# Kernel optimization log

Measured on AMD Instinct MI355X. Metric: run time of the kernel, lower is better.

The kernel has to match this reference:

```python
import jax, jax.numpy as jnp
import numpy as np

# dims: B=4 batch, S=2048 seq, D=4096 in, O=4096 out, E=16 adapters, R=16 rank

def setup_inputs() -> dict:
    key = jax.random.key(0)
    k = jax.random.split(key, 6)
    x = jax.random.normal(k[0], (4, 2048, 4096), jnp.float32)
    W = jax.random.normal(k[1], (4096, 4096), jnp.float32) * 0.02   # base_linear.weight [O, D]
    bias = jax.random.normal(k[2], (4096,), jnp.float32) * 0.02
    A = jax.random.normal(k[3], (16, 16, 4096), jnp.float32) * 0.02  # stacked a_factors [E, R, D]
    Bf = jax.random.normal(k[4], (16, 4096, 16), jnp.float32) * 0.02 # stacked b_factors [E, O, R]
    coeffs = jax.random.uniform(k[5], (16,), jnp.float32)            # task coefficients per adapter
    scales = jnp.full((16,), 0.5, jnp.float32)                       # per-adapter static scales
    return {"x": x, "W": W, "bias": bias, "A": A, "Bf": Bf, "coeffs": coeffs, "scales": scales}

def reference(x, W, bias, A, Bf, coeffs, scales):
    # base: out = x @ W.T + bias
    out = jnp.einsum('bsd,od->bso', x, W) + bias
    # fused LoRA: sum_e coeffs[e]*scales[e] * (x @ A[e].T) @ Bf[e].T
    xa = jnp.einsum('bsd,erd->ebsr', x, A)          # [E, B, S, R] (small: R=16)
    w = coeffs * scales                               # [E]
    upd = jnp.einsum('ebsr,eor,e->bso', xa, Bf, w)  # weighted accumulate over adapters
    return out + upd
```

## Files before the change

### kernel.cpp

```cpp
#include <hip/hip_runtime.h>

typedef float f32x4 __attribute__((ext_vector_type(4)));
typedef __bf16 bf16x8 __attribute__((ext_vector_type(8)));
typedef unsigned short u16x8 __attribute__((ext_vector_type(8)));

__device__ __forceinline__ unsigned short f2bf(float f) {
  union { float f; unsigned int u; } v; v.f = f;
  unsigned int u = v.u;
  unsigned int r = (u + 0x7FFFu + ((u >> 16) & 1u)) >> 16;
  return (unsigned short)r;
}

__global__ __launch_bounds__(256) void k_cast_bf16(const float* __restrict__ in,
                                                   unsigned short* __restrict__ out, int n8) {
  const f32x4* p = (const f32x4*)in;
  for (int i = blockIdx.x * 256 + threadIdx.x; i < n8; i += 2048 * 256) {
    f32x4 a = p[2 * i], b = p[2 * i + 1];
    u16x8 o;
    o[0] = f2bf(a[0]); o[1] = f2bf(a[1]); o[2] = f2bf(a[2]); o[3] = f2bf(a[3]);
    o[4] = f2bf(b[0]); o[5] = f2bf(b[1]); o[6] = f2bf(b[2]); o[7] = f2bf(b[3]);
    ((u16x8*)out)[i] = o;
  }
}

__global__ void k_build_bw(const float* __restrict__ Bf,
                           const float* __restrict__ coeffs,
                           const float* __restrict__ scales,
                           unsigned short* __restrict__ bw) {
  int t = blockIdx.x * 256 + threadIdx.x;
  int o = t >> 8, k = t & 255, e = k >> 4, r = k & 15;
  float v = coeffs[e] * scales[e] * Bf[((size_t)e * 4096 + o) * 16 + r];
  bw[t] = f2bf(v);
}

__global__ void k_build_at(const float* __restrict__ A,
                           unsigned short* __restrict__ at) {
  __shared__ float tile[64][65];
  int kt = blockIdx.x * 64, dt = blockIdx.y * 64;
  int tx = threadIdx.x & 63, ty = threadIdx.x >> 6;
#pragma unroll
  for (int j = 0; j < 64; j += 4)
    tile[ty + j][tx] = A[(size_t)(kt + ty + j) * 4096 + dt + tx];
  __syncthreads();
#pragma unroll
  for (int j = 0; j < 64; j += 4)
    at[(size_t)(dt + ty + j) * 256 + kt + tx] = f2bf(tile[tx][ty + j]);
}

template <int M_, int N_, int K_>
__global__ __launch_bounds__(256) void k_gemm_prep(
    const unsigned short* __restrict__ Abuf,
    const unsigned short* __restrict__ Bbuf,
    const float* __restrict__ Wadd,
    unsigned short* __restrict__ outB) {
  constexpr int NBN = N_ / 128;
  constexpr int NWG = (M_ / 128) * NBN;
  const int bid = blockIdx.x;
  const int swz = (bid & 7) * (NWG / 8) + (bid >> 3);
  const int bm = swz / NBN, bn = swz % NBN;

  __shared__ unsigned short ldsA[128 * 64];
  __shared__ unsigned short ldsB[128 * 64];

  const int t = threadIdx.x, w = t >> 6, l = t & 63;
  const int wr = w >> 1, wc = w & 1;

  f32x4 acc[4][4] = {};
  const int m0 = bm * 128, n0 = bn * 128;
  const int srow = w * 8 + (l >> 3);
  const int scol = (l & 7) * 8;
  const unsigned short* gA = Abuf + (size_t)(m0 + srow) * K_ + scol;
  const unsigned short* gB = Bbuf + (size_t)(n0 + srow) * K_ + scol;

  for (int kt = 0; kt < K_; kt += 64) {
#pragma unroll
    for (int i = 0; i < 4; ++i) {
      __builtin_amdgcn_global_load_lds(
          (__attribute__((address_space(1))) void*)(gA + (size_t)i * 32 * K_ + kt),
          (__attribute__((address_space(3))) void*)(ldsA + i * 2048 + w * 512), 16, 0, 0);
      __builtin_amdgcn_global_load_lds(
          (__attribute__((address_space(1))) void*)(gB + (size_t)i * 32 * K_ + kt),
          (__attribute__((address_space(3))) void*)(ldsB + i * 2048 + w * 512), 16, 0, 0);
    }
    __syncthreads();
#pragma unroll
    for (int kk = 0; kk < 2; ++kk) {
      const int col = kk * 32 + (l >> 4) * 8;
      const int arow = wr * 64 + (l & 15);
      const int brow = wc * 64 + (l & 15);
      bf16x8 af[4], bfv[4];
#pragma unroll
      for (int mi = 0; mi < 4; ++mi)
        af[mi] = *(const bf16x8*)&ldsA[(arow + mi * 16) * 64 + col];
#pragma unroll
      for (int ni = 0; ni < 4; ++ni)
        bfv[ni] = *(const bf16x8*)&ldsB[(brow + ni * 16) * 64 + col];
#pragma unroll
      for (int mi = 0; mi < 4; ++mi)
#pragma unroll
        for (int ni = 0; ni < 4; ++ni)
          acc[mi][ni] = __builtin_amdgcn_mfma_f32_16x16x32_bf16(
              af[mi], bfv[ni], acc[mi][ni], 0, 0, 0);
    }
    __syncthreads();
  }

  const int mrow0 = m0 + wr * 64 + (l >> 4) * 4;
  const int ncol0 = n0 + wc * 64 + (l & 15);
#pragma unroll
  for (int mi = 0; mi < 4; ++mi)
#pragma unroll
    for (int r = 0; r < 4; ++r) {
      const int m = mrow0 + mi * 16 + r;
#pragma unroll
      for (int ni = 0; ni < 4; ++ni) {
        const int n = ncol0 + ni * 16;
        outB[(size_t)m * N_ + n] = f2bf(acc[mi][ni][r] + Wadd[(size_t)m * N_ + n]);
      }
    }
}

template <int M_, int N_, int K_>
__global__ __launch_bounds__(512, 2) void k_gemm256(
    const unsigned short* __restrict__ Abuf,
    const unsigned short* __restrict__ Bbuf,
    const float* __restrict__ bias,
    float* __restrict__ outF) {
  constexpr int NBN = N_ / 256;
  constexpr int NWG = (M_ / 256) * NBN;
  constexpr int NT = K_ / 32;
  static_assert(NWG % 8 == 0, "bijective xcd swizzle");
  static_assert(NT % 2 == 0 && NT >= 6, "pipeline depth");

  const int bid = blockIdx.x;
  const int swz = (bid & 7) * (NWG / 8) + (bid >> 3);
  const int bm = swz / NBN, bn = swz % NBN;
  const int m0 = bm * 256, n0 = bn * 256;

  __shared__ __attribute__((aligned(128))) unsigned short lds[81920];
  char* ldsb = (char*)lds;

  const int tid = threadIdx.x, w = tid >> 6, l = tid & 63;
  const int wr = w >> 2, wc = w & 3;

  const int scol = ((l & 3) ^ ((l >> 3) & 3)) * 8;
  const unsigned short* gA = Abuf + (size_t)(m0 + w * 16 + (l >> 2)) * K_ + scol;
  const unsigned short* gB = Bbuf + (size_t)(n0 + w * 16 + (l >> 2)) * K_ + scol;
  const int dA = w * 1024;
  const int dB = 16384 + w * 1024;

  const int qp = ((l >> 4) ^ ((l >> 1) & 3)) << 4;
  const int raOff = (wr * 128 + (l & 15)) * 64 + qp;
  const int rbOff = 16384 + (wc * 64 + (l & 15)) * 64 + qp;

  f32x4 acc[8][4] = {};

#define STAGE_T(tt, bf)                                                               \
  do {                                                                                \
    const int bb_ = (bf) * 32768;                                                     \
    const size_t ko_ = (size_t)(tt) * 32;                                             \
    _Pragma("unroll") for (int i_ = 0; i_ < 2; ++i_) {                                \
      __builtin_amdgcn_global_load_lds(                                               \
          (__attribute__((address_space(1))) void*)(gA + (size_t)i_ * 128 * K_ + ko_),\
          (__attribute__((address_space(3))) void*)(ldsb + bb_ + i_ * 8192 + dA),     \
          16, 0, 0);                                                                  \
      __builtin_amdgcn_global_load_lds(                                               \
          (__attribute__((address_space(1))) void*)(gB + (size_t)i_ * 128 * K_ + ko_),\
          (__attribute__((address_space(3))) void*)(ldsb + bb_ + i_ * 8192 + dB),     \
          16, 0, 0);                                                                  \
    }                                                                                 \
  } while (0)

#define RD_A(mi, bf) (*(const bf16x8*)(ldsb + (bf) * 32768 + raOff + (mi) * 1024))
#define RD_B(ni, bf) (*(const bf16x8*)(ldsb + (bf) * 32768 + rbOff + (ni) * 1024))

#define TILE_BODY(bf, stg_t, stg_b, do_stg)                                           \
  do {                                                                                \
    bf16x8 fa0 = RD_A(0, bf), fa1 = RD_A(1, bf), fa2 = RD_A(2, bf), fa3 = RD_A(3, bf);\
    bf16x8 fa4 = RD_A(4, bf), fa5 = RD_A(5, bf), fa6 = RD_A(6, bf), fa7 = RD_A(7, bf);\
    bf16x8 fb0 = RD_B(0, bf), fb1 = RD_B(1, bf), fb2 = RD_B(2, bf), fb3 = RD_B(3, bf);\
    if (do_stg) STAGE_T(stg_t, stg_b);                                                \
    __builtin_amdgcn_s_setprio(1);                                                    \
    _Pragma("unroll") for (int ni_ = 0; ni_ < 4; ++ni_) {                             \
      bf16x8 vv = (ni_ == 0) ? fb0 : (ni_ == 1) ? fb1 : (ni_ == 2) ? fb2 : fb3;       \
      acc[0][ni_] = __builtin_amdgcn_mfma_f32_16x16x32_bf16(fa0, vv, acc[0][ni_], 0, 0, 0); \
      acc[1][ni_] = __builtin_amdgcn_mfma_f32_16x16x32_bf16(fa1, vv, acc[1][ni_], 0, 0, 0); \
      acc[2][ni_] = __builtin_amdgcn_mfma_f32_16x16x32_bf16(fa2, vv, acc[2][ni_], 0, 0, 0); \
      acc[3][ni_] = __builtin_amdgcn_mfma_f32_16x16x32_bf16(fa3, vv, acc[3][ni_], 0, 0, 0); \
      acc[4][ni_] = __builtin_amdgcn_mfma_f32_16x16x32_bf16(fa4, vv, acc[4][ni_], 0, 0, 0); \
      acc[5][ni_] = __builtin_amdgcn_mfma_f32_16x16x32_bf16(fa5, vv, acc[5][ni_], 0, 0, 0); \
      acc[6][ni_] = __builtin_amdgcn_mfma_f32_16x16x32_bf16(fa6, vv, acc[6][ni_], 0, 0, 0); \
      acc[7][ni_] = __builtin_amdgcn_mfma_f32_16x16x32_bf16(fa7, vv, acc[7][ni_], 0, 0, 0); \
    }                                                                                 \
    __builtin_amdgcn_s_setprio(0);                                                    \
  } while (0)

  STAGE_T(0, 0); STAGE_T(1, 1); STAGE_T(2, 2);

  int bT = 0;
  for (int tt = 0; tt < NT; tt += 2) {
    const int b0 = bT;
    const int b1 = (bT + 1 >= 5) ? bT + 1 - 5 : bT + 1;
    const int s3 = (bT + 3 >= 5) ? bT + 3 - 5 : bT + 3;
    const int s4 = (bT + 4 >= 5) ? bT + 4 - 5 : bT + 4;
    const bool st3 = (tt + 3) < NT, st4 = (tt + 4) < NT;

    if (tt + 2 < NT) asm volatile("s_waitcnt vmcnt(4)" ::: "memory");
    else             asm volatile("s_waitcnt vmcnt(0)" ::: "memory");
    __builtin_amdgcn_s_barrier();
    __builtin_amdgcn_sched_barrier(0);

    if ((w & 1) == 0) {
      TILE_BODY(b0, tt + 3, s3, st3);
      TILE_BODY(b1, tt + 4, s4, st4);
    } else {
      TILE_BODY(b1, tt + 3, s3, st3);
      TILE_BODY(b0, tt + 4, s4, st4);
    }

    bT += 2; if (bT >= 5) bT -= 5;
  }
#undef STAGE_T
#undef RD_A
#undef RD_B
#undef TILE_BODY

#pragma unroll
  for (int ni = 0; ni < 4; ++ni) {
    const int n = n0 + wc * 64 + ni * 16 + (l & 15);
    const float bv2 = bias[n];
#pragma unroll
    for (int mi = 0; mi < 8; ++mi) {
      const int m = m0 + wr * 128 + mi * 16 + (l >> 4) * 4;
#pragma unroll
      for (int r = 0; r < 4; ++r)
        outF[(size_t)(m + r) * N_ + n] = acc[mi][ni][r] + bv2;
    }
  }
}

extern "C" void kernel_launch(void* const* d_in, const int* in_sizes, int n_in,
                              void* d_out, int out_size, void* d_ws, size_t ws_size,
                              hipStream_t stream) {
  const float* x      = (const float*)d_in[0];
  const float* W      = (const float*)d_in[1];
  const float* bias   = (const float*)d_in[2];
  const float* A      = (const float*)d_in[3];
  const float* Bf     = (const float*)d_in[4];
  const float* coeffs = (const float*)d_in[5];
  const float* scales = (const float*)d_in[6];
  float* out = (float*)d_out;

  char* ws = (char*)d_ws;
  unsigned short* xb   = (unsigned short*)(ws);
  unsigned short* weff = (unsigned short*)(ws + 67108864);
  unsigned short* bw   = (unsigned short*)(ws + 67108864 + 33554432);
  unsigned short* at   = (unsigned short*)(ws + 67108864 + 33554432 + 2097152);

  k_cast_bf16<<<2048, 256, 0, stream>>>(x, xb, (8192 * 4096) / 8);
  k_build_bw<<<4096, 256, 0, stream>>>(Bf, coeffs, scales, bw);
  k_build_at<<<dim3(4, 64), 256, 0, stream>>>(A, at);
  k_gemm_prep<4096, 4096, 256><<<1024, 256, 0, stream>>>(bw, at, W, weff);
  k_gemm256<8192, 4096, 4096><<<512, 512, 0, stream>>>(xb, weff, bias, out);
}
```

Before: 352.3 us.

## Software-pipeline LDS fragment reads against MFMA groups within the K loop

Each tile's compute is split into two MFMA half-groups (low and high A rows), and the LDS fragment reads for the next half are interleaved with the MFMAs of the previous half. The second half of each tile is carried across the barrier into the next iteration, with a prologue and an epilogue added. Scheduling barriers pin this order. The aim is to hide LDS read latency behind matrix-core work instead of loading all fragments before any MFMA. The per-wave odd/even tile order swap is removed, and extra fragment registers are held live, which may raise register pressure at two waves per SIMD.

```diff
diff --git a/kernel.cpp b/kernel.cpp
--- a/kernel.cpp
+++ b/kernel.cpp
@@ -130,7 +130,7 @@
   constexpr int NWG = (M_ / 256) * NBN;
   constexpr int NT = K_ / 32;
   static_assert(NWG % 8 == 0, "bijective xcd swizzle");
-  static_assert(NT % 2 == 0 && NT >= 6, "pipeline depth");
+  static_assert(NT % 2 == 0 && NT >= 8, "pipeline depth");
 
   const int bid = blockIdx.x;
   const int swz = (bid & 7) * (NWG / 8) + (bid >> 3);
@@ -154,6 +154,7 @@
   const int rbOff = 16384 + (wc * 64 + (l & 15)) * 64 + qp;
 
   f32x4 acc[8][4] = {};
+  bf16x8 faL[4], faH[4], fbX[4], fbY[4];
 
 #define STAGE_T(tt, bf)                                                               \
   do {                                                                                \
@@ -173,57 +174,99 @@
 
 #define RD_A(mi, bf) (*(const bf16x8*)(ldsb + (bf) * 32768 + raOff + (mi) * 1024))
 #define RD_B(ni, bf) (*(const bf16x8*)(ldsb + (bf) * 32768 + rbOff + (ni) * 1024))
-
-#define TILE_BODY(bf, stg_t, stg_b, do_stg)                                           \
-  do {                                                                                \
-    bf16x8 fa0 = RD_A(0, bf), fa1 = RD_A(1, bf), fa2 = RD_A(2, bf), fa3 = RD_A(3, bf);\
-    bf16x8 fa4 = RD_A(4, bf), fa5 = RD_A(5, bf), fa6 = RD_A(6, bf), fa7 = RD_A(7, bf);\
-    bf16x8 fb0 = RD_B(0, bf), fb1 = RD_B(1, bf), fb2 = RD_B(2, bf), fb3 = RD_B(3, bf);\
-    if (do_stg) STAGE_T(stg_t, stg_b);                                                \
-    __builtin_amdgcn_s_setprio(1);                                                    \
-    _Pragma("unroll") for (int ni_ = 0; ni_ < 4; ++ni_) {                             \
-      bf16x8 vv = (ni_ == 0) ? fb0 : (ni_ == 1) ? fb1 : (ni_ == 2) ? fb2 : fb3;       \
-      acc[0][ni_] = __builtin_amdgcn_mfma_f32_16x16x32_bf16(fa0, vv, acc[0][ni_], 0, 0, 0); \
-      acc[1][ni_] = __builtin_amdgcn_mfma_f32_16x16x32_bf16(fa1, vv, acc[1][ni_], 0, 0, 0); \
-      acc[2][ni_] = __builtin_amdgcn_mfma_f32_16x16x32_bf16(fa2, vv, acc[2][ni_], 0, 0, 0); \
-      acc[3][ni_] = __builtin_amdgcn_mfma_f32_16x16x32_bf16(fa3, vv, acc[3][ni_], 0, 0, 0); \
-      acc[4][ni_] = __builtin_amdgcn_mfma_f32_16x16x32_bf16(fa4, vv, acc[4][ni_], 0, 0, 0); \
-      acc[5][ni_] = __builtin_amdgcn_mfma_f32_16x16x32_bf16(fa5, vv, acc[5][ni_], 0, 0, 0); \
-      acc[6][ni_] = __builtin_amdgcn_mfma_f32_16x16x32_bf16(fa6, vv, acc[6][ni_], 0, 0, 0); \
-      acc[7][ni_] = __builtin_amdgcn_mfma_f32_16x16x32_bf16(fa7, vv, acc[7][ni_], 0, 0, 0); \
-    }                                                                                 \
-    __builtin_amdgcn_s_setprio(0);                                                    \
+#define SB __builtin_amdgcn_sched_barrier(0)
+
+#define ALPHA(bf, FB)                                                                 \
+  do {                                                                               \
+    faL[0] = RD_A(0, bf); faL[1] = RD_A(1, bf);                                      \
+    faL[2] = RD_A(2, bf); faL[3] = RD_A(3, bf);                                      \
+    FB[0] = RD_B(0, bf); FB[1] = RD_B(1, bf);                                        \
+    FB[2] = RD_B(2, bf); FB[3] = RD_B(3, bf);                                        \
+    SB;                                                                              \
+  } while (0)
+
+#define BETA(bf, stg_t, stg_b, do_stg)                                               \
+  do {                                                                               \
+    faH[0] = RD_A(4, bf); faH[1] = RD_A(5, bf);                                      \
+    faH[2] = RD_A(6, bf); faH[3] = RD_A(7, bf);                                      \
+    if (do_stg) STAGE_T(stg_t, stg_b);                                               \
+    SB;                                                                              \
+  } while (0)
+
+#define G1(FB)                                                                       \
+  do {                                                                               \
+    __builtin_amdgcn_s_setprio(1);                                                   \
+    _Pragma("unroll") for (int ni_ = 0; ni_ < 4; ++ni_) {                            \
+      acc[0][ni_] = __builtin_amdgcn_mfma_f32_16x16x32_bf16(faL[0], FB[ni_], acc[0][ni_], 0, 0, 0); \
+      acc[1][ni_] = __builtin_amdgcn_mfma_f32_16x16x32_bf16(faL[1], FB[ni_], acc[1][ni_], 0, 0, 0); \
+      acc[2][ni_] = __builtin_amdgcn_mfma_f32_16x16x32_bf16(faL[2], FB[ni_], acc[2][ni_], 0, 0, 0); \
+      acc[3][ni_] = __builtin_amdgcn_mfma_f32_16x16x32_bf16(faL[3], FB[ni_], acc[3][ni_], 0, 0, 0); \
+    }                                                                                \
+    __builtin_amdgcn_s_setprio(0);                                                   \
+    SB;                                                                              \
+  } while (0)
+
+#define G2(FB)                                                                       \
+  do {                                                                               \
+    __builtin_amdgcn_s_setprio(1);                                                   \
+    _Pragma("unroll") for (int ni_ = 0; ni_ < 4; ++ni_) {                            \
+      acc[4][ni_] = __builtin_amdgcn_mfma_f32_16x16x32_bf16(faH[0], FB[ni_], acc[4][ni_], 0, 0, 0); \
+      acc[5][ni_] = __builtin_amdgcn_mfma_f32_16x16x32_bf16(faH[1], FB[ni_], acc[5][ni_], 0, 0, 0); \
+      acc[6][ni_] = __builtin_amdgcn_mfma_f32_16x16x32_bf16(faH[2], FB[ni_], acc[6][ni_], 0, 0, 0); \
+      acc[7][ni_] = __builtin_amdgcn_mfma_f32_16x16x32_bf16(faH[3], FB[ni_], acc[7][ni_], 0, 0, 0); \
+    }                                                                                \
+    __builtin_amdgcn_s_setprio(0);                                                   \
+    SB;                                                                              \
+  } while (0)
+
+#define TOPWAIT(cond)                                                                \
+  do {                                                                               \
+    if (cond) asm volatile("s_waitcnt vmcnt(4)" ::: "memory");                       \
+    else      asm volatile("s_waitcnt vmcnt(0)" ::: "memory");                       \
+    __builtin_amdgcn_s_barrier();                                                    \
+    SB;                                                                              \
   } while (0)
 
   STAGE_T(0, 0); STAGE_T(1, 1); STAGE_T(2, 2);
 
-  int bT = 0;
-  for (int tt = 0; tt < NT; tt += 2) {
+  TOPWAIT(2 < NT);
+  ALPHA(0, fbX);
+  BETA(0, 3, 3, 3 < NT);
+  G1(fbX);
+  ALPHA(1, fbY);
+  G2(fbX);
+  BETA(1, 4, 4, 4 < NT);
+  G1(fbY);
+
+  int bT = 2;
+  for (int tt = 2; tt < NT; tt += 2) {
     const int b0 = bT;
     const int b1 = (bT + 1 >= 5) ? bT + 1 - 5 : bT + 1;
     const int s3 = (bT + 3 >= 5) ? bT + 3 - 5 : bT + 3;
     const int s4 = (bT + 4 >= 5) ? bT + 4 - 5 : bT + 4;
-    const bool st3 = (tt + 3) < NT, st4 = (tt + 4) < NT;
-
-    if (tt + 2 < NT) asm volatile("s_waitcnt vmcnt(4)" ::: "memory");
-    else             asm volatile("s_waitcnt vmcnt(0)" ::: "memory");
-    __builtin_amdgcn_s_barrier();
-    __builtin_amdgcn_sched_barrier(0);
-
-    if ((w & 1) == 0) {
-      TILE_BODY(b0, tt + 3, s3, st3);
-      TILE_BODY(b1, tt + 4, s4, st4);
-    } else {
-      TILE_BODY(b1, tt + 3, s3, st3);
-      TILE_BODY(b0, tt + 4, s4, st4);
-    }
+
+    TOPWAIT(tt + 2 < NT);
+    ALPHA(b0, fbX);
+    G2(fbY);
+    BETA(b0, tt + 3, s3, (tt + 3) < NT);
+    G1(fbX);
+    ALPHA(b1, fbY);
+    G2(fbX);
+    BETA(b1, tt + 4, s4, (tt + 4) < NT);
+    G1(fbY);
 
     bT += 2; if (bT >= 5) bT -= 5;
   }
+  G2(fbY);
 #undef STAGE_T
 #undef RD_A
 #undef RD_B
-#undef TILE_BODY
+#undef SB
+#undef ALPHA
+#undef BETA
+#undef G1
+#undef G2
+#undef TOPWAIT
 
 #pragma unroll
   for (int ni = 0; ni < 4; ++ni) {
```

Measured after the change: 346.0 us. Within noise of the previous version (-1.8%).

## Run main GEMM with 16 waves per block and merge small prep kernels

Applied to the files above, without the earlier changes.

The 256x256 GEMM block now uses 1024 threads (16 waves in a 4x4 grid), and each wave computes a 64x64 sub-tile instead of 128x64. Staging needs one load per matrix per thread, and the wait count and per-wave buffer ordering are adjusted to match. The intent is more waves to hide latency and fewer accumulator registers per wave, at the cost of extra LDS fragment reads per MFMA and lower occupancy per CU. The x cast becomes one element-group per thread instead of a grid-stride loop, and the Bw and A-transpose prep kernels are merged into one launch to cut launch overhead.

```diff
diff --git a/kernel.cpp b/kernel.cpp
--- a/kernel.cpp
+++ b/kernel.cpp
@@ -13,38 +13,40 @@
 
 __global__ __launch_bounds__(256) void k_cast_bf16(const float* __restrict__ in,
                                                    unsigned short* __restrict__ out, int n8) {
+  int i = blockIdx.x * 256 + threadIdx.x;
+  if (i >= n8) return;
   const f32x4* p = (const f32x4*)in;
-  for (int i = blockIdx.x * 256 + threadIdx.x; i < n8; i += 2048 * 256) {
-    f32x4 a = p[2 * i], b = p[2 * i + 1];
-    u16x8 o;
-    o[0] = f2bf(a[0]); o[1] = f2bf(a[1]); o[2] = f2bf(a[2]); o[3] = f2bf(a[3]);
-    o[4] = f2bf(b[0]); o[5] = f2bf(b[1]); o[6] = f2bf(b[2]); o[7] = f2bf(b[3]);
-    ((u16x8*)out)[i] = o;
-  }
-}
-
-__global__ void k_build_bw(const float* __restrict__ Bf,
-                           const float* __restrict__ coeffs,
-                           const float* __restrict__ scales,
-                           unsigned short* __restrict__ bw) {
-  int t = blockIdx.x * 256 + threadIdx.x;
-  int o = t >> 8, k = t & 255, e = k >> 4, r = k & 15;
-  float v = coeffs[e] * scales[e] * Bf[((size_t)e * 4096 + o) * 16 + r];
-  bw[t] = f2bf(v);
-}
-
-__global__ void k_build_at(const float* __restrict__ A,
-                           unsigned short* __restrict__ at) {
+  f32x4 a = p[2 * i], b = p[2 * i + 1];
+  u16x8 o;
+  o[0] = f2bf(a[0]); o[1] = f2bf(a[1]); o[2] = f2bf(a[2]); o[3] = f2bf(a[3]);
+  o[4] = f2bf(b[0]); o[5] = f2bf(b[1]); o[6] = f2bf(b[2]); o[7] = f2bf(b[3]);
+  ((u16x8*)out)[i] = o;
+}
+
+__global__ void k_build_bwat(const float* __restrict__ Bf,
+                             const float* __restrict__ coeffs,
+                             const float* __restrict__ scales,
+                             const float* __restrict__ A,
+                             unsigned short* __restrict__ bw,
+                             unsigned short* __restrict__ at) {
   __shared__ float tile[64][65];
-  int kt = blockIdx.x * 64, dt = blockIdx.y * 64;
-  int tx = threadIdx.x & 63, ty = threadIdx.x >> 6;
-#pragma unroll
-  for (int j = 0; j < 64; j += 4)
-    tile[ty + j][tx] = A[(size_t)(kt + ty + j) * 4096 + dt + tx];
-  __syncthreads();
-#pragma unroll
-  for (int j = 0; j < 64; j += 4)
-    at[(size_t)(dt + ty + j) * 256 + kt + tx] = f2bf(tile[tx][ty + j]);
+  if (blockIdx.x < 4096) {
+    int t = blockIdx.x * 256 + threadIdx.x;
+    int o = t >> 8, k = t & 255, e = k >> 4, r = k & 15;
+    float v = coeffs[e] * scales[e] * Bf[((size_t)e * 4096 + o) * 16 + r];
+    bw[t] = f2bf(v);
+  } else {
+    int b = blockIdx.x - 4096;
+    int kt = (b & 3) * 64, dt = (b >> 2) * 64;
+    int tx = threadIdx.x & 63, ty = threadIdx.x >> 6;
+#pragma unroll
+    for (int j = 0; j < 64; j += 4)
+      tile[ty + j][tx] = A[(size_t)(kt + ty + j) * 4096 + dt + tx];
+    __syncthreads();
+#pragma unroll
+    for (int j = 0; j < 64; j += 4)
+      at[(size_t)(dt + ty + j) * 256 + kt + tx] = f2bf(tile[tx][ty + j]);
+  }
 }
 
 template <int M_, int N_, int K_>
@@ -121,7 +123,7 @@
 }
 
 template <int M_, int N_, int K_>
-__global__ __launch_bounds__(512, 2) void k_gemm256(
+__global__ __launch_bounds__(1024) void k_gemm256(
     const unsigned short* __restrict__ Abuf,
     const unsigned short* __restrict__ Bbuf,
     const float* __restrict__ bias,
@@ -150,25 +152,21 @@
   const int dB = 16384 + w * 1024;
 
   const int qp = ((l >> 4) ^ ((l >> 1) & 3)) << 4;
-  const int raOff = (wr * 128 + (l & 15)) * 64 + qp;
+  const int raOff = (wr * 64 + (l & 15)) * 64 + qp;
   const int rbOff = 16384 + (wc * 64 + (l & 15)) * 64 + qp;
 
-  f32x4 acc[8][4] = {};
+  f32x4 acc[4][4] = {};
 
 #define STAGE_T(tt, bf)                                                               \
   do {                                                                                \
     const int bb_ = (bf) * 32768;                                                     \
     const size_t ko_ = (size_t)(tt) * 32;                                             \
-    _Pragma("unroll") for (int i_ = 0; i_ < 2; ++i_) {                                \
-      __builtin_amdgcn_global_load_lds(                                               \
-          (__attribute__((address_space(1))) void*)(gA + (size_t)i_ * 128 * K_ + ko_),\
-          (__attribute__((address_space(3))) void*)(ldsb + bb_ + i_ * 8192 + dA),     \
-          16, 0, 0);                                                                  \
-      __builtin_amdgcn_global_load_lds(                                               \
-          (__attribute__((address_space(1))) void*)(gB + (size_t)i_ * 128 * K_ + ko_),\
-          (__attribute__((address_space(3))) void*)(ldsb + bb_ + i_ * 8192 + dB),     \
-          16, 0, 0);                                                                  \
-    }                                                                                 \
+    __builtin_amdgcn_global_load_lds(                                                 \
+        (__attribute__((address_space(1))) void*)(gA + ko_),                          \
+        (__attribute__((address_space(3))) void*)(ldsb + bb_ + dA), 16, 0, 0);        \
+    __builtin_amdgcn_global_load_lds(                                                 \
+        (__attribute__((address_space(1))) void*)(gB + ko_),                          \
+        (__attribute__((address_space(3))) void*)(ldsb + bb_ + dB), 16, 0, 0);        \
   } while (0)
 
 #define RD_A(mi, bf) (*(const bf16x8*)(ldsb + (bf) * 32768 + raOff + (mi) * 1024))
@@ -176,21 +174,17 @@
 
 #define TILE_BODY(bf, stg_t, stg_b, do_stg)                                           \
   do {                                                                                \
-    bf16x8 fa0 = RD_A(0, bf), fa1 = RD_A(1, bf), fa2 = RD_A(2, bf), fa3 = RD_A(3, bf);\
-    bf16x8 fa4 = RD_A(4, bf), fa5 = RD_A(5, bf), fa6 = RD_A(6, bf), fa7 = RD_A(7, bf);\
-    bf16x8 fb0 = RD_B(0, bf), fb1 = RD_B(1, bf), fb2 = RD_B(2, bf), fb3 = RD_B(3, bf);\
+    bf16x8 fa[4], fb[4];                                                              \
+    _Pragma("unroll") for (int i_ = 0; i_ < 4; ++i_) {                                \
+      fa[i_] = RD_A(i_, bf);                                                          \
+      fb[i_] = RD_B(i_, bf);                                                          \
+    }                                                                                 \
     if (do_stg) STAGE_T(stg_t, stg_b);                                                \
     __builtin_amdgcn_s_setprio(1);                                                    \
-    _Pragma("unroll") for (int ni_ = 0; ni_ < 4; ++ni_) {                             \
-      bf16x8 vv = (ni_ == 0) ? fb0 : (ni_ == 1) ? fb1 : (ni_ == 2) ? fb2 : fb3;       \
-      acc[0][ni_] = __builtin_amdgcn_mfma_f32_16x16x32_bf16(fa0, vv, acc[0][ni_], 0, 0, 0); \
-      acc[1][ni_] = __builtin_amdgcn_mfma_f32_16x16x32_bf16(fa1, vv, acc[1][ni_], 0, 0, 0); \
-      acc[2][ni_] = __builtin_amdgcn_mfma_f32_16x16x32_bf16(fa2, vv, acc[2][ni_], 0, 0, 0); \
-      acc[3][ni_] = __builtin_amdgcn_mfma_f32_16x16x32_bf16(fa3, vv, acc[3][ni_], 0, 0, 0); \
-      acc[4][ni_] = __builtin_amdgcn_mfma_f32_16x16x32_bf16(fa4, vv, acc[4][ni_], 0, 0, 0); \
-      acc[5][ni_] = __builtin_amdgcn_mfma_f32_16x16x32_bf16(fa5, vv, acc[5][ni_], 0, 0, 0); \
-      acc[6][ni_] = __builtin_amdgcn_mfma_f32_16x16x32_bf16(fa6, vv, acc[6][ni_], 0, 0, 0); \
-      acc[7][ni_] = __builtin_amdgcn_mfma_f32_16x16x32_bf16(fa7, vv, acc[7][ni_], 0, 0, 0); \
+    _Pragma("unroll") for (int mi_ = 0; mi_ < 4; ++mi_) {                             \
+      _Pragma("unroll") for (int ni_ = 0; ni_ < 4; ++ni_)                             \
+          acc[mi_][ni_] = __builtin_amdgcn_mfma_f32_16x16x32_bf16(                    \
+              fa[mi_], fb[ni_], acc[mi_][ni_], 0, 0, 0);                              \
     }                                                                                 \
     __builtin_amdgcn_s_setprio(0);                                                    \
   } while (0)
@@ -205,18 +199,13 @@
     const int s4 = (bT + 4 >= 5) ? bT + 4 - 5 : bT + 4;
     const bool st3 = (tt + 3) < NT, st4 = (tt + 4) < NT;
 
-    if (tt + 2 < NT) asm volatile("s_waitcnt vmcnt(4)" ::: "memory");
+    if (tt + 2 < NT) asm volatile("s_waitcnt vmcnt(2)" ::: "memory");
     else             asm volatile("s_waitcnt vmcnt(0)" ::: "memory");
     __builtin_amdgcn_s_barrier();
     __builtin_amdgcn_sched_barrier(0);
 
-    if ((w & 1) == 0) {
-      TILE_BODY(b0, tt + 3, s3, st3);
-      TILE_BODY(b1, tt + 4, s4, st4);
-    } else {
-      TILE_BODY(b1, tt + 3, s3, st3);
-      TILE_BODY(b0, tt + 4, s4, st4);
-    }
+    TILE_BODY(b0, tt + 3, s3, st3);
+    TILE_BODY(b1, tt + 4, s4, st4);
 
     bT += 2; if (bT >= 5) bT -= 5;
   }
@@ -230,8 +219,8 @@
     const int n = n0 + wc * 64 + ni * 16 + (l & 15);
     const float bv2 = bias[n];
 #pragma unroll
-    for (int mi = 0; mi < 8; ++mi) {
-      const int m = m0 + wr * 128 + mi * 16 + (l >> 4) * 4;
+    for (int mi = 0; mi < 4; ++mi) {
+      const int m = m0 + wr * 64 + mi * 16 + (l >> 4) * 4;
 #pragma unroll
       for (int r = 0; r < 4; ++r)
         outF[(size_t)(m + r) * N_ + n] = acc[mi][ni][r] + bv2;
@@ -257,9 +246,8 @@
   unsigned short* bw   = (unsigned short*)(ws + 67108864 + 33554432);
   unsigned short* at   = (unsigned short*)(ws + 67108864 + 33554432 + 2097152);
 
-  k_cast_bf16<<<2048, 256, 0, stream>>>(x, xb, (8192 * 4096) / 8);
-  k_build_bw<<<4096, 256, 0, stream>>>(Bf, coeffs, scales, bw);
-  k_build_at<<<dim3(4, 64), 256, 0, stream>>>(A, at);
+  k_cast_bf16<<<16384, 256, 0, stream>>>(x, xb, (8192 * 4096) / 8);
+  k_build_bwat<<<4352, 256, 0, stream>>>(Bf, coeffs, scales, A, bw, at);
   k_gemm_prep<4096, 4096, 256><<<1024, 256, 0, stream>>>(bw, at, W, weff);
-  k_gemm256<8192, 4096, 4096><<<512, 512, 0, stream>>>(xb, weff, bias, out);
-}
+  k_gemm256<8192, 4096, 4096><<<512, 1024, 0, stream>>>(xb, weff, bias, out);
+}
```

Result: faster. 338.2 us (median of 2 runs) (-4.0%).
